# Kernel tuning notes

Hardware: AMD Instinct MI355X
Metric: run time of the kernel (lower is better)

## Reference

```python
import jax, jax.numpy as jnp
import numpy as np


def setup_inputs() -> dict:
    key = jax.random.key(0)
    k1, k2, k3 = jax.random.split(key, 3)
    B, N, D = 8, 4096, 64
    q = jax.random.normal(k1, (B, N, D), dtype=jnp.float32)
    k = jax.random.normal(k2, (B, N, D), dtype=jnp.float32)
    v = jax.random.normal(k3, (B, N, D), dtype=jnp.float32)
    attn_mask = jnp.ones((B, N), dtype=jnp.int32)  # 1 = attend, 0 = padding
    return {"q": q, "k": k, "v": v, "attn_mask": attn_mask}


def reference(q, k, v, attn_mask):
    # q: [B, n_q, d], k/v: [B, n_k, d], attn_mask: [B, n_k]
    d = q.shape[-1]
    n_q, n_k = q.shape[1], k.shape[1]
    scale = jnp.sqrt(jnp.asarray(d, dtype=q.dtype))
    # [B, n_q, n_k] attention logits
    logits = jnp.einsum("bqd,bkd->bqk", q, k) / scale
    # causal (mask_future=True): tril keep-mask over (n_q, n_k)
    causal = jnp.tril(jnp.ones((n_q, n_k), dtype=bool))
    neg_inf = jnp.asarray(-jnp.inf, dtype=logits.dtype)
    logits = jnp.where(causal[None, :, :], logits, neg_inf)
    # padding mask broadcast over query dim: [B, 1, n_k]
    logits = jnp.where(attn_mask[:, None, :] == 0, neg_inf, logits)
    w = jax.nn.softmax(logits, axis=-1)
    return jnp.einsum("bqk,bkd->bqd", w, v)
```

## Files before the change

### kernel.cpp

```cpp
#include <hip/hip_runtime.h>


#define BATCH 8
#define SEQ   4096
#define DIM   64
#define QT    64
#define NKT   (SEQ / 64)

typedef __attribute__((ext_vector_type(8))) short bf16x8;
typedef __attribute__((ext_vector_type(4))) float f32x4;
typedef __attribute__((ext_vector_type(4))) unsigned u32x4;

__device__ inline short f2bf(float f) {
    unsigned u = __builtin_bit_cast(unsigned, f);
    u += 0x7FFFu + ((u >> 16) & 1u);
    return (short)(u >> 16);
}

__device__ inline unsigned pk2bf(float a, float b) {
    unsigned ua = __builtin_bit_cast(unsigned, a) + 0x8000u;
    unsigned ub = __builtin_bit_cast(unsigned, b) + 0x8000u;
    return __builtin_amdgcn_perm(ub, ua, 0x07060302u);
}

__device__ inline float fast_exp2(float x) {
#if __has_builtin(__builtin_amdgcn_exp2f)
    return __builtin_amdgcn_exp2f(x);
#else
    return exp2f(x);
#endif
}

__device__ inline void gl_lds16(const void* g, void* l) {
    __builtin_amdgcn_global_load_lds(
        (const __attribute__((address_space(1))) void*)g,
        (__attribute__((address_space(3))) void*)l, 16, 0, 0);
}

__device__ inline void nts(float* p, float v) {
    __builtin_nontemporal_store(v, p);
}
__device__ inline void nts4(float* p, f32x4 v) {
    __builtin_nontemporal_store(v, (f32x4*)p);
}
__device__ inline f32x4 ntl4(const float* p) {
    return __builtin_nontemporal_load((const f32x4*)p);
}

__global__ __launch_bounds__(256)
void prep_kv(const float* __restrict__ kg, const float* __restrict__ vg,
             const int* __restrict__ mg, short* __restrict__ kw,
             short* __restrict__ vw, float* __restrict__ mf) {
    const int tile = blockIdx.x;
    const float* kp = kg + (size_t)tile * 64 * DIM;
    const float* vp = vg + (size_t)tile * 64 * DIM;
    short* ko = kw + (size_t)tile * 4096;
    short* vo = vw + (size_t)tile * 4096;
    const int t = threadIdx.x;
    if (mf && t < 64) {
        const int* mp = mg + (size_t)tile * 64;
        mf[(size_t)tile * 64 + t] = mp[t] ? 0.0f : -1e30f;
    }
#pragma unroll
    for (int i = 0; i < 4; ++i) {
        const int flat = i * 256 + t;
        const int key = flat >> 4, d0 = (flat & 15) * 4;
        const f32x4 kv = ntl4(kp + (size_t)key * DIM + d0);
        uint2 kpk;
        kpk.x = pk2bf(kv[0], kv[1]); kpk.y = pk2bf(kv[2], kv[3]);
        *(uint2*)(ko + (((d0 >> 3) << 6) + key) * 8 + (d0 & 7)) = kpk;
        const f32x4 vv = ntl4(vp + (size_t)key * DIM + d0);
        const int vcell = ((key >> 5) << 2) | ((key >> 2) & 3);
        const int vj    = (((key >> 4) & 1) << 2) | (key & 3);
        vo[((vcell << 6) + d0 + 0) * 8 + vj] = f2bf(vv[0]);
        vo[((vcell << 6) + d0 + 1) * 8 + vj] = f2bf(vv[1]);
        vo[((vcell << 6) + d0 + 2) * 8 + vj] = f2bf(vv[2]);
        vo[((vcell << 6) + d0 + 3) * 8 + vj] = f2bf(vv[3]);
    }
}

__global__ __launch_bounds__(512, 8)
void attn_split4(const float* __restrict__ qg, float* __restrict__ og,
                 const short* __restrict__ kw, const short* __restrict__ vw,
                 const float* __restrict__ mf, float* __restrict__ opart,
                 float* __restrict__ lpart) {
    __shared__ __align__(16) char smem[32768];
    short* KbS = (short*)smem;
    short* VbS = (short*)(smem + 16384);
    float* OX = (float*)smem;
    float* LB = (float*)(smem + 16384);

    const int t    = threadIdx.x;
    const int w    = t >> 6;
    const int L    = t & 63;
    const int c15  = L & 15;
    const int quad = L >> 4;
    const int qsub = w & 3;
    const int kh   = w >> 2;

    const int id  = blockIdx.x;
    const int b   = id & 7;
    const int r_  = id >> 3;
    const int j   = r_ & 31;
    const int ch  = r_ >> 5;
    const int nL  = 64 - j;
    const int qLt = 63 - j;

    const float* qp  = qg + (size_t)b * SEQ * DIM;
    const float* mb  = mf + (size_t)b * SEQ;
    const short* kwb = kw + (size_t)b * NKT * 4096;
    const short* vwb = vw + (size_t)b * NKT * 4096;
    float* osl = opart + (size_t)(b * 32 + j) * 12288;
    float* lsl = lpart + (size_t)(b * 32 + j) * 384;
    const float qscale = 0.125f * 1.44269504088896340736f;

    auto stage = [&](int bs, int kt) {
        const short* ks = kwb + (size_t)kt * 4096;
        const short* vs = vwb + (size_t)kt * 4096;
        const int off = w << 9;
        gl_lds16(ks + off + (L << 3), KbS + bs * 4096 + off);
        gl_lds16(vs + off + (L << 3), VbS + bs * 4096 + off);
    };

    bf16x8 vones;
#pragma unroll
    for (int z = 0; z < 8; ++z) vones[z] = (short)0x3F80;

    int sqt[2], sk0[2], sk1[2], smode[2], sos[2], sls[2], nseg;
    sos[0] = sos[1] = 0; sls[0] = sls[1] = 0;
    if (ch == 0) {
        nseg = 1;
        sqt[0] = qLt; sk0[0] = 0;  sk1[0] = 16; smode[0] = 0; sls[0] = 0;
    } else if (ch == 1) {
        nseg = 1;
        sqt[0] = qLt; sk0[0] = 16; sk1[0] = 32; smode[0] = 1; sos[0] = 0; sls[0] = 1;
    } else if (ch == 2) {
        if (nL >= 48) {
            nseg = 1;
            sqt[0] = qLt; sk0[0] = 32; sk1[0] = 48; smode[0] = 1; sos[0] = 1; sls[0] = 2;
        } else {
            nseg = 2;
            sqt[0] = qLt; sk0[0] = 32; sk1[0] = nL;      smode[0] = 1; sos[0] = 1; sls[0] = 2;
            sqt[1] = j;   sk0[1] = 0;  sk1[1] = 48 - nL; smode[1] = 0; sls[1] = 4;
        }
    } else {
        if (nL > 48) {
            nseg = 2;
            sqt[0] = qLt; sk0[0] = 48; sk1[0] = nL;    smode[0] = 1; sos[0] = 2; sls[0] = 3;
            sqt[1] = j;   sk0[1] = 0;  sk1[1] = j + 1; smode[1] = 2;
        } else if (nL == 48) {
            nseg = 1;
            sqt[0] = j; sk0[0] = 0; sk1[0] = j + 1; smode[0] = 2;
        } else {
            nseg = 1;
            sqt[0] = j; sk0[0] = 48 - nL; sk1[0] = j + 1; smode[0] = 1; sos[0] = 2; sls[0] = 5;
        }
    }

    for (int seg = 0; seg < nseg; ++seg) {
        const int qt   = sqt[seg];
        const int kt0  = sk0[seg];
        const int kt1  = sk1[seg];
        const int mode = smode[seg];

        const int qbase = qt * QT;
        const int qrow  = qbase + qsub * 16 + c15;

        bf16x8 Qf[2];
#pragma unroll
        for (int c = 0; c < 2; ++c) {
            const float* src = qp + (size_t)qrow * DIM + c * 32 + quad * 8;
            float4 x = *(const float4*)(src);
            float4 y = *(const float4*)(src + 4);
            bf16x8 f;
            f[0] = f2bf(x.x * qscale); f[1] = f2bf(x.y * qscale);
            f[2] = f2bf(x.z * qscale); f[3] = f2bf(x.w * qscale);
            f[4] = f2bf(y.x * qscale); f[5] = f2bf(y.y * qscale);
            f[6] = f2bf(y.z * qscale); f[7] = f2bf(y.w * qscale);
            Qf[c] = f;
        }

        f32x4 lacc = (f32x4){0.f, 0.f, 0.f, 0.f};
        f32x4 Oacc[4];
#pragma unroll
        for (int nb = 0; nb < 4; ++nb) Oacc[nb] = (f32x4){0.f, 0.f, 0.f, 0.f};

        stage(0, kt0);

        for (int kt = kt0; kt < kt1; ++kt) {
            const int cur = (kt - kt0) & 1;
            __syncthreads();
            if (kt + 1 < kt1) stage(cur ^ 1, kt + 1);

            const short* Kt = KbS + cur * 4096;
            const short* Vt = VbS + cur * 4096;

            const float4 ma0 = *(const float4*)&mb[kt * 64 + (2 * kh + 0) * 16 + quad * 4];
            const float4 ma1 = *(const float4*)&mb[kt * 64 + (2 * kh + 1) * 16 + quad * 4];

            f32x4 sacc[2];
            sacc[0] = (f32x4){0.f, 0.f, 0.f, 0.f};
            sacc[1] = (f32x4){0.f, 0.f, 0.f, 0.f};
#pragma unroll
            for (int c = 0; c < 2; ++c) {
#pragma unroll
                for (int i = 0; i < 2; ++i) {
                    bf16x8 kf = *(const bf16x8*)&Kt[(((quad + 4 * c) << 6) + (2 * kh + i) * 16 + c15) * 8];
                    sacc[i] = __builtin_amdgcn_mfma_f32_16x16x32_bf16(kf, Qf[c], sacc[i], 0, 0, 0);
                }
            }

            const bool diag = (kt == qt);
            unsigned pu[4];
#pragma unroll
            for (int i = 0; i < 2; ++i) {
                const int kb = 2 * kh + i;
                const float4 ma = i ? ma1 : ma0;
                const float mar[4] = {ma.x, ma.y, ma.z, ma.w};
                float p[4];
#pragma unroll
                for (int r = 0; r < 4; ++r) {
                    float s = sacc[i][r] + mar[r];
                    if (diag) {
                        const int keyg = kt * 64 + kb * 16 + quad * 4 + r;
                        if (keyg > qrow) s = -1e30f;
                    }
                    p[r] = fast_exp2(fminf(s, 80.0f));
                }
                pu[2 * i]     = pk2bf(p[0], p[1]);
                pu[2 * i + 1] = pk2bf(p[2], p[3]);
            }

            const bf16x8 pf = __builtin_bit_cast(bf16x8,
                (u32x4){pu[0], pu[1], pu[2], pu[3]});
#pragma unroll
            for (int nb = 0; nb < 4; ++nb) {
                bf16x8 vf = *(const bf16x8*)&Vt[(((kh * 4 + quad) << 6) + nb * 16 + c15) * 8];
                Oacc[nb] = __builtin_amdgcn_mfma_f32_16x16x32_bf16(pf, vf, Oacc[nb], 0, 0, 0);
            }
            lacc = __builtin_amdgcn_mfma_f32_16x16x32_bf16(pf, vones, lacc, 0, 0, 0);
        }

        __syncthreads();
        if (w >= 4) {
            const int g = w & 3;
#pragma unroll
            for (int r = 0; r < 4; ++r) {
                const int q = quad * 4 + r;
#pragma unroll
                for (int nb = 0; nb < 4; ++nb)
                    OX[(g * 16 + q) * 64 + nb * 16 + c15] = Oacc[nb][r];
            }
            if (c15 == 0) {
#pragma unroll
                for (int r = 0; r < 4; ++r)
                    LB[g * 16 + quad * 4 + r] = lacc[r];
            }
        }
        __syncthreads();
        if (w < 4) {
            float lt_[4], inv_[4];
#pragma unroll
            for (int r = 0; r < 4; ++r) {
                lt_[r]  = lacc[r] + LB[w * 16 + quad * 4 + r];
                inv_[r] = 1.0f / lt_[r];
            }
            float* dst = (mode == 1) ? osl + (size_t)sos[seg] * 4096
                                     : og + ((size_t)b * SEQ + qbase) * DIM;
            if (mode != 2 && c15 == 0) {
#pragma unroll
                for (int r = 0; r < 4; ++r)
                    nts(&lsl[sls[seg] * 64 + w * 16 + quad * 4 + r], lt_[r]);
            }
#pragma unroll
            for (int r = 0; r < 4; ++r) {
                const float ir = (mode == 2) ? inv_[r] : 1.0f;
                const int rl = w * 16 + quad * 4 + r;
#pragma unroll
                for (int nb = 0; nb < 4; ++nb)
                    nts(&dst[(size_t)rl * DIM + nb * 16 + c15],
                        (Oacc[nb][r] + OX[rl * 64 + nb * 16 + c15]) * ir);
            }
        }
        __syncthreads();
    }
}

__global__ __launch_bounds__(256)
void merge4(float* __restrict__ og, const float* __restrict__ opart,
            const float* __restrict__ lpart) {
    const int id = blockIdx.x;
    const int b = id & 7, j = id >> 3;
    const int nL = 64 - j, qLt = 63 - j;
    const float* os = opart + (size_t)(b * 32 + j) * 12288;
    const float* ls = lpart + (size_t)(b * 32 + j) * 384;
    const int t = threadIdx.x;
    const bool has3 = (nL > 48);

    float* opL = og + ((size_t)b * SEQ + (size_t)qLt * 64) * DIM;
#pragma unroll
    for (int i = 0; i < 4; ++i) {
        const int flat = i * 256 + t;
        const int row = flat >> 4;
        const int c4  = (flat & 15) * 4;
        float l = ls[row] + ls[64 + row] + ls[128 + row];
        if (has3) l += ls[192 + row];
        const float inv = 1.0f / l;
        const f32x4 a  = ntl4(opL + (size_t)row * DIM + c4);
        const f32x4 p0 = ntl4(os + (size_t)row * 64 + c4);
        const f32x4 p1 = ntl4(os + 4096 + (size_t)row * 64 + c4);
        f32x4 s = a + p0 + p1;
        if (has3) s = s + ntl4(os + 8192 + (size_t)row * 64 + c4);
        nts4(opL + (size_t)row * DIM + c4, s * inv);
    }

    if (nL < 48) {
        float* opS = og + ((size_t)b * SEQ + (size_t)j * 64) * DIM;
#pragma unroll
        for (int i = 0; i < 4; ++i) {
            const int flat = i * 256 + t;
            const int row = flat >> 4;
            const int c4  = (flat & 15) * 4;
            const float inv = 1.0f / (ls[256 + row] + ls[320 + row]);
            const f32x4 a  = ntl4(opS + (size_t)row * DIM + c4);
            const f32x4 p2 = ntl4(os + 8192 + (size_t)row * 64 + c4);
            nts4(opS + (size_t)row * DIM + c4, (a + p2) * inv);
        }
    }
}

template <bool WS>
__global__ __launch_bounds__(512, 4)
void attn_fwd(const float* __restrict__ qg, const float* __restrict__ kg,
              const float* __restrict__ vg, const int* __restrict__ mg,
              float* __restrict__ og, const short* __restrict__ kw,
              const short* __restrict__ vw) {
    __shared__ __align__(16) char smem[59392];
    short* KbS = (short*)smem;
    short* VbS = (short*)(smem + 16384);
    float* Ml  = (float*)(smem + 43008);
    float* OX = (float*)smem;
    float* LB = (float*)(smem + 16384);

    const int t    = threadIdx.x;
    const int w    = t >> 6;
    const int L    = t & 63;
    const int c15  = L & 15;
    const int quad = L >> 4;
    const int qsub = w & 3;
    const int kh   = w >> 2;

    const int id = blockIdx.x;
    const int b  = id & 7;
    const int j  = id >> 3;
    const int qb = (j < 32) ? (63 - j) : (j - 32);
    const int qbase  = qb * QT;
    const int ntiles = qb + 1;

    const float* qp = qg + (size_t)b * SEQ * DIM;
    const float* kp = kg + (size_t)b * SEQ * DIM;
    const float* vp = vg + (size_t)b * SEQ * DIM;
    const int*   mp = mg + (size_t)b * SEQ;
    const short* kwb = WS ? kw + (size_t)b * NKT * 4096 : nullptr;
    const short* vwb = WS ? vw + (size_t)b * NKT * 4096 : nullptr;

    const int qrow = qbase + qsub * 16 + c15;
    const float qscale = 0.125f * 1.44269504088896340736f;

    bf16x8 Qf[2];
#pragma unroll
    for (int c = 0; c < 2; ++c) {
        const float* src = qp + (size_t)qrow * DIM + c * 32 + quad * 8;
        float4 x = *(const float4*)(src);
        float4 y = *(const float4*)(src + 4);
        bf16x8 f;
        f[0] = f2bf(x.x * qscale); f[1] = f2bf(x.y * qscale);
        f[2] = f2bf(x.z * qscale); f[3] = f2bf(x.w * qscale);
        f[4] = f2bf(y.x * qscale); f[5] = f2bf(y.y * qscale);
        f[6] = f2bf(y.z * qscale); f[7] = f2bf(y.w * qscale);
        Qf[c] = f;
    }

    auto stage = [&](int bs, int kt) {
        const short* ks = kwb + (size_t)kt * 4096;
        const short* vs = vwb + (size_t)kt * 4096;
        const int off = w << 9;
        gl_lds16(ks + off + (L << 3), KbS + bs * 4096 + off);
        gl_lds16(vs + off + (L << 3), VbS + bs * 4096 + off);
    };

    for (int i = t; i < ntiles * 64; i += 512)
        Ml[i] = mp[i] ? 0.0f : -1e30f;

    float lsum = 0.0f;
    f32x4 Oacc[4];
#pragma unroll
    for (int nb = 0; nb < 4; ++nb) Oacc[nb] = (f32x4){0.f, 0.f, 0.f, 0.f};

    if constexpr (WS) stage(0, 0);

    for (int kt = 0; kt < ntiles; ++kt) {
        const int cur = WS ? (kt & 1) : 0;

        if constexpr (!WS) {
            __syncthreads();
#pragma unroll
            for (int it = 0; it < 2; ++it) {
                const int flat = it * 512 + t;
                const int key = flat >> 4, d0 = (flat & 15) * 4;
                const float4 kv = *(const float4*)(kp + (size_t)(kt * 64 + key) * DIM + d0);
                uint2 kk;
                kk.x = pk2bf(kv.x, kv.y); kk.y = pk2bf(kv.z, kv.w);
                *(uint2*)&KbS[(((d0 >> 3) << 6) + key) * 8 + (d0 & 7)] = kk;
                const float4 vv = *(const float4*)(vp + (size_t)(kt * 64 + key) * DIM + d0);
                const int vcell = ((key >> 5) << 2) | ((key >> 2) & 3);
                const int vj    = (((key >> 4) & 1) << 2) | (key & 3);
                VbS[((vcell << 6) + d0 + 0) * 8 + vj] = f2bf(vv.x);
                VbS[((vcell << 6) + d0 + 1) * 8 + vj] = f2bf(vv.y);
                VbS[((vcell << 6) + d0 + 2) * 8 + vj] = f2bf(vv.z);
                VbS[((vcell << 6) + d0 + 3) * 8 + vj] = f2bf(vv.w);
            }
            __syncthreads();
        } else {
            __syncthreads();
            if (kt + 1 < ntiles) stage(cur ^ 1, kt + 1);
        }

        const short* Kt = KbS + cur * 4096;
        const short* Vt = VbS + cur * 4096;

        f32x4 sacc[2];
        sacc[0] = (f32x4){0.f, 0.f, 0.f, 0.f};
        sacc[1] = (f32x4){0.f, 0.f, 0.f, 0.f};
#pragma unroll
        for (int c = 0; c < 2; ++c) {
#pragma unroll
            for (int i = 0; i < 2; ++i) {
                bf16x8 kf = *(const bf16x8*)&Kt[(((quad + 4 * c) << 6) + (2 * kh + i) * 16 + c15) * 8];
                sacc[i] = __builtin_amdgcn_mfma_f32_16x16x32_bf16(kf, Qf[c], sacc[i], 0, 0, 0);
            }
        }

        const bool diag = (kt == ntiles - 1);
        unsigned pu[4];
#pragma unroll
        for (int i = 0; i < 2; ++i) {
            const int kb = 2 * kh + i;
            const float4 ma = *(const float4*)&Ml[kt * 64 + kb * 16 + quad * 4];
            const float mar[4] = {ma.x, ma.y, ma.z, ma.w};
            float p[4];
#pragma unroll
            for (int r = 0; r < 4; ++r) {
                float s = sacc[i][r] + mar[r];
                if (diag) {
                    const int keyg = kt * 64 + kb * 16 + quad * 4 + r;
                    if (keyg > qrow) s = -1e30f;
                }
                p[r] = fast_exp2(fminf(s, 80.0f));
                lsum += p[r];
            }
            pu[2 * i]     = pk2bf(p[0], p[1]);
            pu[2 * i + 1] = pk2bf(p[2], p[3]);
        }

        const bf16x8 pf = __builtin_bit_cast(bf16x8,
            (u32x4){pu[0], pu[1], pu[2], pu[3]});
#pragma unroll
        for (int nb = 0; nb < 4; ++nb) {
            bf16x8 vf = *(const bf16x8*)&Vt[(((kh * 4 + quad) << 6) + nb * 16 + c15) * 8];
            Oacc[nb] = __builtin_amdgcn_mfma_f32_16x16x32_bf16(pf, vf, Oacc[nb], 0, 0, 0);
        }
    }

    lsum += __shfl_xor(lsum, 16);
    lsum += __shfl_xor(lsum, 32);

    __syncthreads();
    if (w >= 4) {
        const int g = w & 3;
#pragma unroll
        for (int r = 0; r < 4; ++r) {
            const int q = quad * 4 + r;
#pragma unroll
            for (int nb = 0; nb < 4; ++nb)
                OX[(g * 16 + q) * 64 + nb * 16 + c15] = Oacc[nb][r];
        }
        if (quad == 0) LB[g * 16 + c15] = lsum;
    }
    __syncthreads();
    if (w < 4) {
        const float inv = 1.0f / (lsum + LB[w * 16 + c15]);
        float* op = og + (size_t)b * SEQ * DIM;
#pragma unroll
        for (int r = 0; r < 4; ++r) {
            const float ir = __shfl(inv, (L & 48) + ((L & 48) >> 2) + r);
            const int row = qbase + w * 16 + quad * 4 + r;
#pragma unroll
            for (int nb = 0; nb < 4; ++nb)
                op[(size_t)row * DIM + nb * 16 + c15] =
                    (Oacc[nb][r] + OX[(w * 16 + quad * 4 + r) * 64 + nb * 16 + c15]) * ir;
        }
    }
}

extern "C" void kernel_launch(void* const* d_in, const int* in_sizes, int n_in,
                              void* d_out, int out_size, void* d_ws, size_t ws_size,
                              hipStream_t stream) {
    (void)in_sizes; (void)n_in; (void)out_size;
    const float* q = (const float*)d_in[0];
    const float* k = (const float*)d_in[1];
    const float* v = (const float*)d_in[2];
    const int*   m = (const int*)d_in[3];
    float* o = (float*)d_out;

    const size_t kvB    = (size_t)BATCH * NKT * 4096 * sizeof(short);
    const size_t maddB  = (size_t)BATCH * SEQ * sizeof(float);
    const size_t opartB = (size_t)BATCH * 32 * 12288 * sizeof(float);
    const size_t lpartB = (size_t)BATCH * 32 * 384 * sizeof(float);
    const size_t need4  = 2 * kvB + maddB + opartB + lpartB;

    if (ws_size >= need4) {
        short* kw = (short*)d_ws;
        short* vw = kw + (size_t)BATCH * NKT * 4096;
        float* mf = (float*)((char*)d_ws + 2 * kvB);
        float* opart = (float*)((char*)d_ws + 2 * kvB + maddB);
        float* lpart = opart + (size_t)BATCH * 32 * 12288;
        prep_kv<<<dim3(BATCH * NKT), 256, 0, stream>>>(k, v, m, kw, vw, mf);
        attn_split4<<<dim3(1024), 512, 0, stream>>>(q, o, kw, vw, mf, opart, lpart);
        merge4<<<dim3(256), 256, 0, stream>>>(o, opart, lpart);
    } else if (ws_size >= 2 * kvB) {
        short* kw = (short*)d_ws;
        short* vw = kw + (size_t)BATCH * NKT * 4096;
        prep_kv<<<dim3(BATCH * NKT), 256, 0, stream>>>(k, v, m, kw, vw, nullptr);
        attn_fwd<true><<<dim3(512), 512, 0, stream>>>(q, k, v, m, o, kw, vw);
    } else {
        attn_fwd<false><<<dim3(512), 512, 0, stream>>>(q, k, v, m, o, nullptr, nullptr);
    }
}
```

Before: 132.8 us.

## Tune split attention loop: manual barrier, mask-in-accumulator, setprio, plain stores

Replaces __syncthreads with an explicit vmcnt wait plus s_barrier, and folds the padding mask into the initial score accumulator. It drops the fminf clamp before exp2 and interleaves the K and V buffers per stage. It also wraps the MFMA blocks in s_setprio, lowers launch bounds occupancy from 8 to 4, and swaps nontemporal loads and stores for ordinary ones in the split and merge kernels. These changes target barrier and issue overhead, but removing the clamp risks overflow if scores exceed the exp2 range.

After: 125.0 us. -5.9%, faster.

```diff
diff --git a/kernel.cpp b/kernel.cpp
--- a/kernel.cpp
+++ b/kernel.cpp
@@ -37,12 +37,6 @@
         (__attribute__((address_space(3))) void*)l, 16, 0, 0);
 }
 
-__device__ inline void nts(float* p, float v) {
-    __builtin_nontemporal_store(v, p);
-}
-__device__ inline void nts4(float* p, f32x4 v) {
-    __builtin_nontemporal_store(v, (f32x4*)p);
-}
 __device__ inline f32x4 ntl4(const float* p) {
     return __builtin_nontemporal_load((const f32x4*)p);
 }
@@ -79,14 +73,13 @@
     }
 }
 
-__global__ __launch_bounds__(512, 8)
+__global__ __launch_bounds__(512, 4)
 void attn_split4(const float* __restrict__ qg, float* __restrict__ og,
                  const short* __restrict__ kw, const short* __restrict__ vw,
                  const float* __restrict__ mf, float* __restrict__ opart,
                  float* __restrict__ lpart) {
     __shared__ __align__(16) char smem[32768];
     short* KbS = (short*)smem;
-    short* VbS = (short*)(smem + 16384);
     float* OX = (float*)smem;
     float* LB = (float*)(smem + 16384);
 
@@ -118,8 +111,9 @@
         const short* ks = kwb + (size_t)kt * 4096;
         const short* vs = vwb + (size_t)kt * 4096;
         const int off = w << 9;
-        gl_lds16(ks + off + (L << 3), KbS + bs * 4096 + off);
-        gl_lds16(vs + off + (L << 3), VbS + bs * 4096 + off);
+        short* base = KbS + bs * 8192;
+        gl_lds16(ks + off + (L << 3), base + off);
+        gl_lds16(vs + off + (L << 3), base + 4096 + off);
     };
 
     bf16x8 vones;
@@ -179,6 +173,7 @@
             f[6] = f2bf(y.z * qscale); f[7] = f2bf(y.w * qscale);
             Qf[c] = f;
         }
+        asm volatile("" ::: "memory");
 
         f32x4 lacc = (f32x4){0.f, 0.f, 0.f, 0.f};
         f32x4 Oacc[4];
@@ -186,21 +181,28 @@
         for (int nb = 0; nb < 4; ++nb) Oacc[nb] = (f32x4){0.f, 0.f, 0.f, 0.f};
 
         stage(0, kt0);
+        int cur = 0;
+        const float* mrow = mb + (size_t)kt0 * 64 + (2 * kh) * 16 + quad * 4;
 
         for (int kt = kt0; kt < kt1; ++kt) {
-            const int cur = (kt - kt0) & 1;
-            __syncthreads();
+            asm volatile("s_waitcnt vmcnt(0)" ::: "memory");
+            __builtin_amdgcn_s_barrier();
+            asm volatile("" ::: "memory");
+
+            const float4 ma0 = *(const float4*)(mrow);
+            const float4 ma1 = *(const float4*)(mrow + 16);
+            mrow += 64;
+            asm volatile("" ::: "memory");
             if (kt + 1 < kt1) stage(cur ^ 1, kt + 1);
 
-            const short* Kt = KbS + cur * 4096;
-            const short* Vt = VbS + cur * 4096;
-
-            const float4 ma0 = *(const float4*)&mb[kt * 64 + (2 * kh + 0) * 16 + quad * 4];
-            const float4 ma1 = *(const float4*)&mb[kt * 64 + (2 * kh + 1) * 16 + quad * 4];
+            const short* Kt = KbS + cur * 8192;
+            const short* Vt = Kt + 4096;
+            cur ^= 1;
 
             f32x4 sacc[2];
-            sacc[0] = (f32x4){0.f, 0.f, 0.f, 0.f};
-            sacc[1] = (f32x4){0.f, 0.f, 0.f, 0.f};
+            sacc[0] = (f32x4){ma0.x, ma0.y, ma0.z, ma0.w};
+            sacc[1] = (f32x4){ma1.x, ma1.y, ma1.z, ma1.w};
+            __builtin_amdgcn_s_setprio(1);
 #pragma unroll
             for (int c = 0; c < 2; ++c) {
 #pragma unroll
@@ -209,23 +211,21 @@
                     sacc[i] = __builtin_amdgcn_mfma_f32_16x16x32_bf16(kf, Qf[c], sacc[i], 0, 0, 0);
                 }
             }
+            __builtin_amdgcn_s_setprio(0);
 
             const bool diag = (kt == qt);
             unsigned pu[4];
 #pragma unroll
             for (int i = 0; i < 2; ++i) {
-                const int kb = 2 * kh + i;
-                const float4 ma = i ? ma1 : ma0;
-                const float mar[4] = {ma.x, ma.y, ma.z, ma.w};
                 float p[4];
 #pragma unroll
                 for (int r = 0; r < 4; ++r) {
-                    float s = sacc[i][r] + mar[r];
+                    float s = sacc[i][r];
                     if (diag) {
-                        const int keyg = kt * 64 + kb * 16 + quad * 4 + r;
+                        const int keyg = kt * 64 + (2 * kh + i) * 16 + quad * 4 + r;
                         if (keyg > qrow) s = -1e30f;
                     }
-                    p[r] = fast_exp2(fminf(s, 80.0f));
+                    p[r] = fast_exp2(s);
                 }
                 pu[2 * i]     = pk2bf(p[0], p[1]);
                 pu[2 * i + 1] = pk2bf(p[2], p[3]);
@@ -233,12 +233,14 @@
 
             const bf16x8 pf = __builtin_bit_cast(bf16x8,
                 (u32x4){pu[0], pu[1], pu[2], pu[3]});
+            __builtin_amdgcn_s_setprio(1);
 #pragma unroll
             for (int nb = 0; nb < 4; ++nb) {
                 bf16x8 vf = *(const bf16x8*)&Vt[(((kh * 4 + quad) << 6) + nb * 16 + c15) * 8];
                 Oacc[nb] = __builtin_amdgcn_mfma_f32_16x16x32_bf16(pf, vf, Oacc[nb], 0, 0, 0);
             }
             lacc = __builtin_amdgcn_mfma_f32_16x16x32_bf16(pf, vones, lacc, 0, 0, 0);
+            __builtin_amdgcn_s_setprio(0);
         }
 
         __syncthreads();
@@ -270,7 +272,7 @@
             if (mode != 2 && c15 == 0) {
 #pragma unroll
                 for (int r = 0; r < 4; ++r)
-                    nts(&lsl[sls[seg] * 64 + w * 16 + quad * 4 + r], lt_[r]);
+                    lsl[sls[seg] * 64 + w * 16 + quad * 4 + r] = lt_[r];
             }
 #pragma unroll
             for (int r = 0; r < 4; ++r) {
@@ -278,8 +280,8 @@
                 const int rl = w * 16 + quad * 4 + r;
 #pragma unroll
                 for (int nb = 0; nb < 4; ++nb)
-                    nts(&dst[(size_t)rl * DIM + nb * 16 + c15],
-                        (Oacc[nb][r] + OX[rl * 64 + nb * 16 + c15]) * ir);
+                    dst[(size_t)rl * DIM + nb * 16 + c15] =
+                        (Oacc[nb][r] + OX[rl * 64 + nb * 16 + c15]) * ir;
             }
         }
         __syncthreads();
@@ -306,12 +308,20 @@
         float l = ls[row] + ls[64 + row] + ls[128 + row];
         if (has3) l += ls[192 + row];
         const float inv = 1.0f / l;
-        const f32x4 a  = ntl4(opL + (size_t)row * DIM + c4);
-        const f32x4 p0 = ntl4(os + (size_t)row * 64 + c4);
-        const f32x4 p1 = ntl4(os + 4096 + (size_t)row * 64 + c4);
-        f32x4 s = a + p0 + p1;
-        if (has3) s = s + ntl4(os + 8192 + (size_t)row * 64 + c4);
-        nts4(opL + (size_t)row * DIM + c4, s * inv);
+        const float4 a  = *(const float4*)(opL + (size_t)row * DIM + c4);
+        const float4 p0 = *(const float4*)(os + (size_t)row * 64 + c4);
+        const float4 p1 = *(const float4*)(os + 4096 + (size_t)row * 64 + c4);
+        float sx = a.x + p0.x + p1.x;
+        float sy = a.y + p0.y + p1.y;
+        float sz = a.z + p0.z + p1.z;
+        float sw = a.w + p0.w + p1.w;
+        if (has3) {
+            const float4 p2 = *(const float4*)(os + 8192 + (size_t)row * 64 + c4);
+            sx += p2.x; sy += p2.y; sz += p2.z; sw += p2.w;
+        }
+        float4 r;
+        r.x = sx * inv; r.y = sy * inv; r.z = sz * inv; r.w = sw * inv;
+        *(float4*)(opL + (size_t)row * DIM + c4) = r;
     }
 
     if (nL < 48) {
@@ -322,9 +332,14 @@
             const int row = flat >> 4;
             const int c4  = (flat & 15) * 4;
             const float inv = 1.0f / (ls[256 + row] + ls[320 + row]);
-            const f32x4 a  = ntl4(opS + (size_t)row * DIM + c4);
-            const f32x4 p2 = ntl4(os + 8192 + (size_t)row * 64 + c4);
-            nts4(opS + (size_t)row * DIM + c4, (a + p2) * inv);
+            const float4 a  = *(const float4*)(opS + (size_t)row * DIM + c4);
+            const float4 p2 = *(const float4*)(os + 8192 + (size_t)row * 64 + c4);
+            float4 r;
+            r.x = (a.x + p2.x) * inv;
+            r.y = (a.y + p2.y) * inv;
+            r.z = (a.z + p2.z) * inv;
+            r.w = (a.w + p2.w) * inv;
+            *(float4*)(opS + (size_t)row * DIM + c4) = r;
         }
     }
 }
```
